# Kernel optimization log

Measured on AMD Instinct MI355X. Metric: run time of the kernel, lower is better.

The kernel has to match this reference:

```python
import jax, jax.numpy as jnp
import numpy as np

KH, KW = 3, 3
STRIDE = (1, 1)
PAD = (1, 1)
DIL = (1, 1)

def _unfold(x, kh, kw, stride, padding, dilation):
    # Faithful torch.nn.functional.unfold: output (B, C*kh*kw, L) with
    # feature ordering channel-slowest, then kh, then kw.
    B, C, H, W = x.shape
    h_out = (H + 2 * padding[0] - dilation[0] * (kh - 1) - 1) // stride[0] + 1
    w_out = (W + 2 * padding[1] - dilation[1] * (kw - 1) - 1) // stride[1] + 1
    xp = jnp.pad(x, ((0, 0), (0, 0), (padding[0], padding[0]), (padding[1], padding[1])))
    rows = []
    for i in range(kh):  # small fixed kernel loop (9 slices), not a data-dim loop
        for j in range(kw):
            r0 = i * dilation[0]
            c0 = j * dilation[1]
            patch = xp[:, :, r0:r0 + h_out * stride[0]:stride[0],
                             c0:c0 + w_out * stride[1]:stride[1]]  # (B,C,h_out,w_out)
            rows.append(patch)
    # stack -> (B, C, kh*kw, h_out, w_out); reorder so feature dim = C*kh*kw
    p = jnp.stack(rows, axis=2)
    p = p.reshape(B, C * kh * kw, h_out * w_out)
    return p, h_out, w_out

def transform_transposed_unfolded_input(inp_unf):
    # Default hook: identity (as in the base class).
    return inp_unf

def reference(x, weight, bias):
    B = x.shape[0]
    O = weight.shape[0]
    inp_unf, h_out, w_out = _unfold(x, KH, KW, STRIDE, PAD, DIL)   # (B, C*k*k, L)
    inp_t = jnp.swapaxes(inp_unf, 1, 2)                            # (B, L, C*k*k)
    inp_t = transform_transposed_unfolded_input(inp_t)
    w2d = weight.reshape(O, -1)                                    # (O, C*k*k)
    out_unf = jnp.einsum('blk,ok->bol', inp_t, w2d)                # (B, O, L)
    out = out_unf.reshape(B, O, h_out, w_out)
    out = out + bias.reshape(1, O, 1, 1)
    return out

def setup_inputs() -> dict:
    key = jax.random.key(0)
    k1, k2, k3 = jax.random.split(key, 3)
    x = jax.random.normal(k1, (32, 128, 56, 56), dtype=jnp.float32)
    fan_in = 128 * KH * KW
    weight = jax.random.normal(k2, (256, 128, KH, KW), dtype=jnp.float32) / np.sqrt(fan_in)
    bias = jax.random.normal(k3, (256,), dtype=jnp.float32) * 0.01
    return {"x": x, "weight": weight, "bias": bias}
```

## Files before the change

kernel.cpp:

```cpp
#include <hip/hip_runtime.h>
#include <hip/hip_bf16.h>
#include <cstdint>

typedef float f32x4 __attribute__((ext_vector_type(4)));
typedef short bf16x8 __attribute__((ext_vector_type(8)));

#define BATCH 32
#define CIN   128
#define HIMG  56
#define WIMG  56
#define HWSZ  3136
#define OCH   256
#define HP    58
#define WP    58

#define BM 128
#define BN 128
#define BK 64
#define NSTEP 18

__global__ void cast_transpose_x(const float* __restrict__ x,
                                 __hip_bfloat16* __restrict__ xb) {
    __shared__ float tile[32][33];
    const int hw0 = blockIdx.x * 32;
    const int c0  = blockIdx.y * 32;
    const int b   = blockIdx.z;
    const int tx  = threadIdx.x;
    const int ty  = threadIdx.y;

    const float* src = x + ((size_t)(b * CIN + c0) * HWSZ) + hw0;
#pragma unroll
    for (int k = 0; k < 4; ++k) {
        int c = ty + k * 8;
        tile[c][tx] = src[(size_t)c * HWSZ + tx];
    }
    __syncthreads();
#pragma unroll
    for (int k = 0; k < 4; ++k) {
        int hwl = ty + k * 8;
        int hw = hw0 + hwl;
        int h = hw / WIMG;
        int w = hw - h * WIMG;
        size_t dst = (((size_t)b * HP + (h + 1)) * WP + (w + 1)) * CIN + c0 + tx;
        xb[dst] = __float2bfloat16(tile[tx][hwl]);
    }
}

__global__ void prep_w(const float* __restrict__ wsrc,
                       __hip_bfloat16* __restrict__ wb) {
    int idx = blockIdx.x * 256 + threadIdx.x;
    int c    = idx & 127;
    int rest = idx >> 7;
    int o    = rest & 255;
    int ij   = rest >> 8;
    wb[idx] = __float2bfloat16(wsrc[((size_t)o * CIN + c) * 9 + ij]);
}

__device__ __forceinline__ void gload16(const void* g, void* l) {
    __builtin_amdgcn_global_load_lds(
        (const __attribute__((address_space(1))) unsigned*)g,
        (__attribute__((address_space(3))) unsigned*)l,
        16, 0, 0);
}

__global__ __launch_bounds__(256, 2)
void conv_gemm(const __hip_bfloat16* __restrict__ xb,
               const __hip_bfloat16* __restrict__ wb,
               const float* __restrict__ bias,
               float* __restrict__ out) {
    __shared__ __attribute__((aligned(16))) char smem[65536];

    const int tid = threadIdx.x;
    const int wv  = tid >> 6;
    const int ln  = tid & 63;

    const int bid = blockIdx.x;
    const int mt  = bid >> 1;
    const int nt  = bid & 1;
    const int m0  = mt * BM;
    const int n0  = nt * BN;

    const int rl = ln >> 3;
    const int cs = ln & 7;
    const int colsrc = ((cs * 16) ^ (rl << 4)) >> 1;

    const __hip_bfloat16* aSrc[4];
    const __hip_bfloat16* bSrc[4];
#pragma unroll
    for (int q = 0; q < 4; ++q) {
        int row = wv * 32 + q * 8 + rl;
        int p  = m0 + row;
        int b  = p / HWSZ;
        int hw = p - b * HWSZ;
        int h  = hw / WIMG;
        int w  = hw - h * WIMG;
        aSrc[q] = xb + (((size_t)b * HP + h) * WP + w) * CIN + colsrc;
        int n = n0 + row;
        bSrc[q] = wb + (size_t)n * CIN + colsrc;
    }
    const int ldst = wv * 4096 + ln * 16;

#define STAGE(buf, s) do {                                             \
        int ij_  = (s) >> 1;                                           \
        int ck0_ = ((s) & 1) << 6;                                     \
        int ii_  = ij_ / 3;                                            \
        int jj_  = ij_ - ii_ * 3;                                      \
        int offA_ = (ii_ * WP + jj_) * CIN + ck0_;                     \
        int offB_ = ij_ * (OCH * CIN) + ck0_;                          \
        char* bA_ = smem + (buf) * 32768;                              \
        char* bB_ = bA_ + 16384;                                       \
        _Pragma("unroll")                                              \
        for (int q_ = 0; q_ < 4; ++q_) {                               \
            gload16(aSrc[q_] + offA_, bA_ + ldst + q_ * 1024);         \
            gload16(bSrc[q_] + offB_, bB_ + ldst + q_ * 1024);         \
        }                                                              \
    } while (0)

    const int wm = wv >> 1, wn = wv & 1;
    const int laneM = ln & 15;
    const int laneK = ln >> 4;
    const int swz   = (laneM & 7) << 4;
    const int arow0 = (wm * 64 + laneM) * 128;
    const int brow0 = (wn * 64 + laneM) * 128;

    f32x4 acc[4][4] = {};

    int cur = 0;
    STAGE(0, 0);

#pragma unroll 2
    for (int s = 0; s < NSTEP; ++s) {
        __syncthreads();
        if (s + 1 < NSTEP) STAGE(cur ^ 1, s + 1);
        const char* baseA = smem + cur * 32768;
        const char* baseB = baseA + 16384;
#pragma unroll
        for (int kk = 0; kk < 2; ++kk) {
            const int kb  = kk * 64 + laneK * 16;
            const int kbs = kb ^ swz;
            bf16x8 af[4], bfr[4];
#pragma unroll
            for (int mi = 0; mi < 4; ++mi)
                af[mi] = *(const bf16x8*)(baseA + arow0 + mi * (16 * 128) + kbs);
#pragma unroll
            for (int ni = 0; ni < 4; ++ni)
                bfr[ni] = *(const bf16x8*)(baseB + brow0 + ni * (16 * 128) + kbs);
#pragma unroll
            for (int mi = 0; mi < 4; ++mi)
#pragma unroll
                for (int ni = 0; ni < 4; ++ni)
                    acc[mi][ni] = __builtin_amdgcn_mfma_f32_16x16x32_bf16(
                        af[mi], bfr[ni], acc[mi][ni], 0, 0, 0);
        }
        cur ^= 1;
    }
#undef STAGE

    const int laneC = ln & 15;
    const int laneR = (ln >> 4) * 4;
    float bn[4];
#pragma unroll
    for (int ni = 0; ni < 4; ++ni)
        bn[ni] = bias[n0 + wn * 64 + ni * 16 + laneC];

#pragma unroll
    for (int mi = 0; mi < 4; ++mi) {
        int p0 = m0 + wm * 64 + mi * 16 + laneR;
        int b  = p0 / HWSZ;
        int hw = p0 - b * HWSZ;
#pragma unroll
        for (int ni = 0; ni < 4; ++ni) {
            int n = n0 + wn * 64 + ni * 16 + laneC;
            float4 v;
            v.x = acc[mi][ni][0] + bn[ni];
            v.y = acc[mi][ni][1] + bn[ni];
            v.z = acc[mi][ni][2] + bn[ni];
            v.w = acc[mi][ni][3] + bn[ni];
            *(float4*)(out + ((size_t)(b * OCH + n) * HWSZ + hw)) = v;
        }
    }
}

extern "C" void kernel_launch(void* const* d_in, const int* in_sizes, int n_in,
                              void* d_out, int out_size, void* d_ws, size_t ws_size,
                              hipStream_t stream) {
    const float* x    = (const float*)d_in[0];
    const float* w    = (const float*)d_in[1];
    const float* bias = (const float*)d_in[2];
    float* out = (float*)d_out;

    char* ws = (char*)d_ws;
    __hip_bfloat16* xbuf = (__hip_bfloat16*)ws;
    __hip_bfloat16* wbuf = (__hip_bfloat16*)(ws + 27557888);

    hipMemsetAsync(xbuf, 0, 27557888, stream);
    cast_transpose_x<<<dim3(98, 4, 32), dim3(32, 8), 0, stream>>>(x, xbuf);
    prep_w<<<9 * 256 * 128 / 256, 256, 0, stream>>>(w, wbuf);
    conv_gemm<<<(100352 / BM) * (OCH / BN), 256, 0, stream>>>(xbuf, wbuf, bias, out);
}
```

Measured before the change: 111.3 us.

## Enlarge GEMM tile to 256x256 with 8 waves, interleaved prefetch, border-only zeroing

The conv GEMM now uses 512-thread blocks, each computing a full 256x256 output tile (all output channels). That doubles A-tile reuse and removes the duplicate input loads made by the two N-tiles. The main loop is split into four MFMA quadrants, with global-to-LDS prefetch chunks interleaved between them, plus explicit barriers, setprio, and an XCD-aware block remap. The full-workspace memset is replaced by a small kernel that zeroes only the padding border. Risks: 128KB of dynamic LDS and 512 threads limit occupancy to roughly one block per CU, and 392 blocks may leave tail imbalance across CUs.

```diff
diff --git a/kernel.cpp b/kernel.cpp
--- a/kernel.cpp
+++ b/kernel.cpp
@@ -5,19 +5,28 @@
 typedef float f32x4 __attribute__((ext_vector_type(4)));
 typedef short bf16x8 __attribute__((ext_vector_type(8)));
 
-#define BATCH 32
 #define CIN   128
-#define HIMG  56
 #define WIMG  56
 #define HWSZ  3136
 #define OCH   256
 #define HP    58
 #define WP    58
-
-#define BM 128
-#define BN 128
-#define BK 64
-#define NSTEP 18
+#define NT    18
+
+__global__ void zero_border(__hip_bfloat16* __restrict__ xb) {
+    int idx = blockIdx.x * 256 + threadIdx.x;
+    int c8  = idx & 15;
+    int t   = idx >> 4;
+    int b   = t / 228;
+    int pos = t - b * 228;
+    int h, w;
+    if (pos < 58)       { h = 0;             w = pos; }
+    else if (pos < 116) { h = 57;            w = pos - 58; }
+    else if (pos < 172) { h = pos - 116 + 1; w = 0; }
+    else                { h = pos - 172 + 1; w = 57; }
+    uint4 z = {0, 0, 0, 0};
+    *(uint4*)((char*)xb + (((size_t)(b * HP + h) * WP + w) * CIN + c8 * 8) * 2) = z;
+}
 
 __global__ void cast_transpose_x(const float* __restrict__ x,
                                  __hip_bfloat16* __restrict__ xb) {
@@ -63,114 +72,146 @@
         16, 0, 0);
 }
 
-__global__ __launch_bounds__(256, 2)
+__global__ __launch_bounds__(512, 2)
 void conv_gemm(const __hip_bfloat16* __restrict__ xb,
                const __hip_bfloat16* __restrict__ wb,
                const float* __restrict__ bias,
                float* __restrict__ out) {
-    __shared__ __attribute__((aligned(16))) char smem[65536];
+    extern __shared__ __attribute__((aligned(16))) char smem[];
 
     const int tid = threadIdx.x;
     const int wv  = tid >> 6;
     const int ln  = tid & 63;
 
-    const int bid = blockIdx.x;
-    const int mt  = bid >> 1;
-    const int nt  = bid & 1;
-    const int m0  = mt * BM;
-    const int n0  = nt * BN;
-
-    const int rl = ln >> 3;
-    const int cs = ln & 7;
-    const int colsrc = ((cs * 16) ^ (rl << 4)) >> 1;
-
-    const __hip_bfloat16* aSrc[4];
-    const __hip_bfloat16* bSrc[4];
+    int bid = blockIdx.x;
+    bid = (bid & 7) * 49 + (bid >> 3);
+    const int m0 = bid * 256;
+
+    const int srow = tid >> 3;
+    const int cs   = tid & 7;
+    const int colsrc = ((cs * 16) ^ ((srow & 7) << 4)) >> 1;
+    int aOff[4], bOff[4];
 #pragma unroll
     for (int q = 0; q < 4; ++q) {
-        int row = wv * 32 + q * 8 + rl;
+        int row = q * 64 + srow;
         int p  = m0 + row;
         int b  = p / HWSZ;
         int hw = p - b * HWSZ;
         int h  = hw / WIMG;
         int w  = hw - h * WIMG;
-        aSrc[q] = xb + (((size_t)b * HP + h) * WP + w) * CIN + colsrc;
-        int n = n0 + row;
-        bSrc[q] = wb + (size_t)n * CIN + colsrc;
-    }
-    const int ldst = wv * 4096 + ln * 16;
-
-#define STAGE(buf, s) do {                                             \
-        int ij_  = (s) >> 1;                                           \
-        int ck0_ = ((s) & 1) << 6;                                     \
-        int ii_  = ij_ / 3;                                            \
-        int jj_  = ij_ - ii_ * 3;                                      \
-        int offA_ = (ii_ * WP + jj_) * CIN + ck0_;                     \
-        int offB_ = ij_ * (OCH * CIN) + ck0_;                          \
-        char* bA_ = smem + (buf) * 32768;                              \
-        char* bB_ = bA_ + 16384;                                       \
-        _Pragma("unroll")                                              \
-        for (int q_ = 0; q_ < 4; ++q_) {                               \
-            gload16(aSrc[q_] + offA_, bA_ + ldst + q_ * 1024);         \
-            gload16(bSrc[q_] + offB_, bB_ + ldst + q_ * 1024);         \
-        }                                                              \
-    } while (0)
-
-    const int wm = wv >> 1, wn = wv & 1;
-    const int laneM = ln & 15;
-    const int laneK = ln >> 4;
-    const int swz   = (laneM & 7) << 4;
-    const int arow0 = (wm * 64 + laneM) * 128;
-    const int brow0 = (wn * 64 + laneM) * 128;
-
-    f32x4 acc[4][4] = {};
-
-    int cur = 0;
-    STAGE(0, 0);
+        aOff[q] = ((b * HP + h) * WP + w) * CIN + colsrc;
+        bOff[q] = row * CIN + colsrc;
+    }
+    const int ldsd = tid * 16;
+
+#define SA(buf,q,offA_) gload16(xb + aOff[q] + (offA_), smem + (buf)*65536 + (q)*8192 + ldsd)
+#define SB(buf,q,offB_) gload16(wb + bOff[q] + (offB_), smem + (buf)*65536 + 32768 + (q)*8192 + ldsd)
+
+    const int wm  = wv >> 2;
+    const int wn  = wv & 3;
+    const int fr  = ln & 15;
+    const int kby = (ln >> 4) * 16;
+    const int swz = (ln & 7) << 4;
+
+    f32x4 acc[8][4] = {};
+    bf16x8 af[4][2], bq0[2][2], bq1[2][2];
+
+#define READ_A(base, mh) do {                                                 \
+    _Pragma("unroll") for (int mi = 0; mi < 4; ++mi)                          \
+    _Pragma("unroll") for (int kk = 0; kk < 2; ++kk)                          \
+        af[mi][kk] = *(const bf16x8*)((base) +                                \
+            (wm*128 + (mh)*64 + mi*16 + fr)*128 + ((kk*64 + kby) ^ swz));     \
+} while (0)
+
+#define READ_B(base, nh, dst) do {                                            \
+    _Pragma("unroll") for (int ni = 0; ni < 2; ++ni)                          \
+    _Pragma("unroll") for (int kk = 0; kk < 2; ++kk)                          \
+        dst[ni][kk] = *(const bf16x8*)((base) + 32768 +                       \
+            (wn*64 + (nh)*32 + ni*16 + fr)*128 + ((kk*64 + kby) ^ swz));      \
+} while (0)
+
+#define MQ(mh, nh, B) do {                                                    \
+    _Pragma("unroll") for (int kk = 0; kk < 2; ++kk)                          \
+    _Pragma("unroll") for (int mi = 0; mi < 4; ++mi)                          \
+    _Pragma("unroll") for (int ni = 0; ni < 2; ++ni)                          \
+        acc[(mh)*4+mi][(nh)*2+ni] = __builtin_amdgcn_mfma_f32_16x16x32_bf16(  \
+            af[mi][kk], B[ni][kk], acc[(mh)*4+mi][(nh)*2+ni], 0, 0, 0);       \
+} while (0)
+
+    SA(0,0,0); SA(0,1,0); SA(0,2,0); SA(0,3,0);
+    SB(0,0,0); SB(0,1,0); SB(0,2,0); SB(0,3,0);
+    asm volatile("s_waitcnt vmcnt(0)" ::: "memory");
+    __builtin_amdgcn_s_barrier();
 
 #pragma unroll 2
-    for (int s = 0; s < NSTEP; ++s) {
-        __syncthreads();
-        if (s + 1 < NSTEP) STAGE(cur ^ 1, s + 1);
-        const char* baseA = smem + cur * 32768;
-        const char* baseB = baseA + 16384;
-#pragma unroll
-        for (int kk = 0; kk < 2; ++kk) {
-            const int kb  = kk * 64 + laneK * 16;
-            const int kbs = kb ^ swz;
-            bf16x8 af[4], bfr[4];
-#pragma unroll
-            for (int mi = 0; mi < 4; ++mi)
-                af[mi] = *(const bf16x8*)(baseA + arow0 + mi * (16 * 128) + kbs);
-#pragma unroll
-            for (int ni = 0; ni < 4; ++ni)
-                bfr[ni] = *(const bf16x8*)(baseB + brow0 + ni * (16 * 128) + kbs);
-#pragma unroll
-            for (int mi = 0; mi < 4; ++mi)
-#pragma unroll
-                for (int ni = 0; ni < 4; ++ni)
-                    acc[mi][ni] = __builtin_amdgcn_mfma_f32_16x16x32_bf16(
-                        af[mi], bfr[ni], acc[mi][ni], 0, 0, 0);
-        }
-        cur ^= 1;
-    }
-#undef STAGE
-
-    const int laneC = ln & 15;
-    const int laneR = (ln >> 4) * 4;
+    for (int t = 0; t < NT; ++t) {
+        const int cur = t & 1;
+        const char* base = smem + cur * 65536;
+        const int  nx = cur ^ 1;
+        const bool pf = (t + 1 < NT);
+        const int s   = t + 1;
+        const int ij  = s >> 1;
+        const int ck0 = (s & 1) << 6;
+        const int ii  = ij / 3;
+        const int jj  = ij - ii * 3;
+        const int offA = (ii * WP + jj) * CIN + ck0;
+        const int offB = ij * (OCH * CIN) + ck0;
+
+        if (pf) { SA(nx,0,offA); SA(nx,1,offA); SA(nx,2,offA); }
+        READ_A(base, 0);
+        READ_B(base, 0, bq0);
+        __builtin_amdgcn_s_barrier();
+        asm volatile("s_waitcnt lgkmcnt(0)" ::: "memory");
+        __builtin_amdgcn_s_setprio(1);
+        MQ(0, 0, bq0);
+        __builtin_amdgcn_s_setprio(0);
+        __builtin_amdgcn_s_barrier();
+
+        if (pf) { SA(nx,3,offA); SB(nx,0,offB); SB(nx,1,offB); }
+        READ_B(base, 1, bq1);
+        __builtin_amdgcn_s_barrier();
+        asm volatile("s_waitcnt lgkmcnt(0)" ::: "memory");
+        __builtin_amdgcn_s_setprio(1);
+        MQ(0, 1, bq1);
+        __builtin_amdgcn_s_setprio(0);
+        __builtin_amdgcn_s_barrier();
+
+        if (pf) { SB(nx,2,offB); SB(nx,3,offB); }
+        READ_A(base, 1);
+        __builtin_amdgcn_s_barrier();
+        asm volatile("s_waitcnt lgkmcnt(0)" ::: "memory");
+        __builtin_amdgcn_s_setprio(1);
+        MQ(1, 1, bq1);
+        __builtin_amdgcn_s_setprio(0);
+        __builtin_amdgcn_s_barrier();
+
+        __builtin_amdgcn_s_setprio(1);
+        MQ(1, 0, bq0);
+        __builtin_amdgcn_s_setprio(0);
+        asm volatile("s_waitcnt vmcnt(0)" ::: "memory");
+        __builtin_amdgcn_s_barrier();
+        __builtin_amdgcn_sched_barrier(0);
+    }
+#undef SA
+#undef SB
+#undef READ_A
+#undef READ_B
+#undef MQ
+
+    const int laneR4 = (ln >> 4) * 4;
     float bn[4];
 #pragma unroll
     for (int ni = 0; ni < 4; ++ni)
-        bn[ni] = bias[n0 + wn * 64 + ni * 16 + laneC];
-
-#pragma unroll
-    for (int mi = 0; mi < 4; ++mi) {
-        int p0 = m0 + wm * 64 + mi * 16 + laneR;
+        bn[ni] = bias[wn * 64 + ni * 16 + fr];
+
+#pragma unroll
+    for (int mi = 0; mi < 8; ++mi) {
+        int p0 = m0 + wm * 128 + mi * 16 + laneR4;
         int b  = p0 / HWSZ;
         int hw = p0 - b * HWSZ;
 #pragma unroll
         for (int ni = 0; ni < 4; ++ni) {
-            int n = n0 + wn * 64 + ni * 16 + laneC;
+            int n = wn * 64 + ni * 16 + fr;
             float4 v;
             v.x = acc[mi][ni][0] + bn[ni];
             v.y = acc[mi][ni][1] + bn[ni];
@@ -193,8 +234,11 @@
     __hip_bfloat16* xbuf = (__hip_bfloat16*)ws;
     __hip_bfloat16* wbuf = (__hip_bfloat16*)(ws + 27557888);
 
-    hipMemsetAsync(xbuf, 0, 27557888, stream);
+    hipFuncSetAttribute(reinterpret_cast<const void*>(conv_gemm),
+                        hipFuncAttributeMaxDynamicSharedMemorySize, 131072);
+
+    zero_border<<<456, 256, 0, stream>>>(xbuf);
     cast_transpose_x<<<dim3(98, 4, 32), dim3(32, 8), 0, stream>>>(x, xbuf);
     prep_w<<<9 * 256 * 128 / 256, 256, 0, stream>>>(w, wbuf);
-    conv_gemm<<<(100352 / BM) * (OCH / BN), 256, 0, stream>>>(xbuf, wbuf, bias, out);
-}
+    conv_gemm<<<392, 512, 131072, stream>>>(xbuf, wbuf, bias, out);
+}
```

Result: faster. 105.1 us (-5.5%).
